# Performance work log

Measured on AMD Instinct MI355X. Metric: run time of the kernel, lower is better.

Reference implementation:

```python
import jax, jax.numpy as jnp
import numpy as np

HEAD = 8
PAD = (2, 2)   # (mod//2, mod//2 + mod%2) for dim=508, head=8 -> mod=4
EPS = 1e-6


def setup_inputs() -> dict:
    key = jax.random.key(0)
    ks = jax.random.split(key, 4)
    d_pad = 512  # 508 + mod(4)
    s = 1.0 / np.sqrt(d_pad).astype(np.float32)
    inp = jax.random.normal(ks[0], (2, 2048, 508), dtype=jnp.float32)
    Wq = jax.random.normal(ks[1], (d_pad, d_pad), dtype=jnp.float32) * s
    Wk = jax.random.normal(ks[2], (d_pad, d_pad), dtype=jnp.float32) * s
    Wv = jax.random.normal(ks[3], (d_pad, d_pad), dtype=jnp.float32) * s
    gamma = jnp.ones((d_pad,), dtype=jnp.float32)
    beta = jnp.zeros((d_pad,), dtype=jnp.float32)
    return {"inp": inp, "Wq": Wq, "Wk": Wk, "Wv": Wv, "gamma": gamma, "beta": beta}


def reference(inp, Wq, Wk, Wv, gamma, beta):
    # pad feature dim so it divides head count (torch F.pad on last dim)
    x = jnp.pad(inp, ((0, 0), (0, 0), (PAD[0], PAD[1])))  # [B, L, D]
    residual = x
    b, l, d = x.shape
    h = HEAD
    dh = d // h
    inv_sqrt_dh = 1.0 / np.sqrt(dh).astype(np.float32)

    def proj(W):
        # torch Linear (no bias): x @ W.T ; then split heads -> [B, H, L, dh]
        return (x @ W.T).reshape(b, l, h, dh).transpose(0, 2, 1, 3)

    q = proj(Wq)
    k = proj(Wk)
    v = proj(Wv)

    score = jnp.einsum('bhld,bhmd->bhlm', q, k) * inv_sqrt_dh  # [B,H,L,L]
    attn = jax.nn.softmax(score, axis=-1)
    out = jnp.einsum('bhlm,bhmd->bhld', attn, v)               # [B,H,L,dh]
    out = out.transpose(0, 2, 1, 3).reshape(b, l, d)           # unshape

    # dropout is identity in eval mode; residual + layernorm
    y = out + residual
    mu = jnp.mean(y, axis=-1, keepdims=True)
    var = jnp.mean(jnp.square(y - mu), axis=-1, keepdims=True)
    z = (y - mu) / jnp.sqrt(var + EPS)
    out = gamma * z + beta

    out = out[:, :, PAD[0]:-PAD[1]]  # strip padding back to original dim
    return out, attn
```

## Files before the change

kernel.cpp:

```cpp
#include <hip/hip_runtime.h>

typedef short bf16x8 __attribute__((ext_vector_type(8)));
typedef float f32x4 __attribute__((ext_vector_type(4)));
typedef unsigned short u16;
typedef u16 u16x8 __attribute__((ext_vector_type(8)));
typedef u16 u16x4 __attribute__((ext_vector_type(4)));

#define L_ 2048
#define D_ 512
#define H_ 8
#define DH_ 64
#define DIN 508

static __device__ __forceinline__ u16 f2b(float f){
  unsigned u = __builtin_bit_cast(unsigned, f);
  unsigned r = u + 0x7fffu + ((u >> 16) & 1u);
  return (u16)(r >> 16);
}
static __device__ __forceinline__ float b2f(u16 u){
  unsigned x = ((unsigned)u) << 16;
  return __builtin_bit_cast(float, x);
}
#define MFMA16(a,b,c) __builtin_amdgcn_mfma_f32_16x16x32_bf16(a,b,c,0,0,0)

__global__ __launch_bounds__(512) void proj_kernel(
    const float* __restrict__ inp, const float* __restrict__ Wq,
    const float* __restrict__ Wk, const float* __restrict__ Wv,
    u16* __restrict__ Qg, u16* __restrict__ Kg, u16* __restrict__ Vt)
{
  __shared__ u16 Xl[128*72];
  __shared__ u16 Wl[128*72];
  const int t = threadIdx.x;
  const int lane = t & 63, wid = t >> 6;
  const int wr = wid >> 2, wc = wid & 3;
  const int i0 = blockIdx.x * 128;
  const int j0 = blockIdx.y * 128;
  const int mat = j0 >> 9;
  const float* __restrict__ W = (mat==0) ? Wq : (mat==1) ? Wk : Wv;
  const int jbase = j0 & 511;
  const int srow = t >> 3, sc8 = (t & 7) * 8;

  f32x4 acc[4][2];
  #pragma unroll
  for (int a=0;a<4;++a){
    #pragma unroll
    for (int bq=0;bq<2;++bq){ f32x4 z = {0.f,0.f,0.f,0.f}; acc[a][bq] = z; }
  }

  for (int kt=0; kt<8; ++kt){
    const int k0 = kt*64;
    __syncthreads();
    #pragma unroll
    for (int it=0; it<2; ++it){
      const int r = srow + 64*it;
      u16x8 xb;
      const int gi = i0 + r;
      #pragma unroll
      for (int e=0;e<8;++e){
        const int k = k0 + sc8 + e;
        float v = (k>=2 && k<510) ? inp[gi*DIN + (k-2)] : 0.f;
        xb[e] = f2b(v);
      }
      *(u16x8*)&Xl[r*72 + sc8] = xb;
      const float* wp = W + (jbase + r)*D_ + k0 + sc8;
      u16x8 wb;
      #pragma unroll
      for (int e=0;e<8;++e) wb[e] = f2b(wp[e]);
      *(u16x8*)&Wl[r*72 + sc8] = wb;
    }
    __syncthreads();
    #pragma unroll
    for (int ks=0; ks<2; ++ks){
      const int ko = ks*32 + (lane>>4)*8;
      bf16x8 af[4], bfr[2];
      #pragma unroll
      for (int fm=0; fm<4; ++fm)
        af[fm] = *(const bf16x8*)&Xl[(wr*64 + fm*16 + (lane&15))*72 + ko];
      #pragma unroll
      for (int fn=0; fn<2; ++fn)
        bfr[fn] = *(const bf16x8*)&Wl[(wc*32 + fn*16 + (lane&15))*72 + ko];
      #pragma unroll
      for (int fm=0; fm<4; ++fm){
        #pragma unroll
        for (int fn=0; fn<2; ++fn)
          acc[fm][fn] = MFMA16(af[fm], bfr[fn], acc[fm][fn]);
      }
    }
  }
  #pragma unroll
  for (int fm=0; fm<4; ++fm){
    const int ibase = i0 + wr*64 + fm*16 + (lane>>4)*4;
    const int b = ibase >> 11;
    const int li = ibase & (L_-1);
    #pragma unroll
    for (int fn=0; fn<2; ++fn){
      const int n = j0 + wc*32 + fn*16 + (lane&15);
      const int h = (n>>6) & 7;
      const int dh = n & 63;
      if (mat == 2){
        u16x4 pk;
        #pragma unroll
        for (int r=0;r<4;++r) pk[r] = f2b(acc[fm][fn][r]);
        *(u16x4*)&Vt[((size_t)(b*H_+h)*DH_ + dh)*L_ + li] = pk;
      } else {
        u16* dst = ((mat==0)? Qg : Kg) + ((size_t)(b*H_+h)*L_ + li)*DH_ + dh;
        #pragma unroll
        for (int r=0;r<4;++r) dst[(size_t)r*DH_] = f2b(acc[fm][fn][r]);
      }
    }
  }
}

__global__ __launch_bounds__(512, 4) void attn_kernel(
    const u16* __restrict__ Qg, const u16* __restrict__ Kg,
    const u16* __restrict__ Vt, float* __restrict__ attn, float* __restrict__ Og)
{
  __shared__ u16 Kl[128*72];
  __shared__ u16 Vl[64*136];
  __shared__ u16 Pt[32*136];
  __shared__ float rsp[8][32];
  __shared__ float inv_rs[32];

  const int t = threadIdx.x, lane = t & 63, wid = t >> 6;
  const int q0 = blockIdx.x * 32;
  const int bh = blockIdx.y;
  const u16* Qp = Qg + ((size_t)bh*L_ + q0)*DH_;
  const u16* Kp = Kg + (size_t)bh*L_*DH_;
  const u16* Vp = Vt + (size_t)bh*DH_*L_;

  bf16x8 qf[2][2];
  #pragma unroll
  for (int qi=0;qi<2;++qi){
    #pragma unroll
    for (int ks=0;ks<2;++ks)
      qf[qi][ks] = *(const bf16x8*)&Qp[(size_t)(qi*16 + (lane&15))*DH_ + ks*32 + (lane>>4)*8];
  }

  const int kr0 = t>>3, kc8 = (t&7)*8;
  const int vr0 = t>>4, vcm = (t&15)*8;
  const int g4 = (lane>>4)*8;
  const int mrow = wid*16 + (lane&15);

  float racc0 = 0.f, racc1 = 0.f;
  u16x8 ka = *(const u16x8*)&Kp[(size_t)kr0*DH_ + kc8];
  u16x8 kb = *(const u16x8*)&Kp[(size_t)(64+kr0)*DH_ + kc8];
  for (int kt=0; kt<16; ++kt){
    __syncthreads();
    *(u16x8*)&Kl[kr0*72 + kc8] = ka;
    *(u16x8*)&Kl[(64+kr0)*72 + kc8] = kb;
    __syncthreads();
    if (kt < 15){
      ka = *(const u16x8*)&Kp[(size_t)((kt+1)*128 + kr0)*DH_ + kc8];
      kb = *(const u16x8*)&Kp[(size_t)((kt+1)*128 + 64 + kr0)*DH_ + kc8];
    }
    bf16x8 kf0 = *(const bf16x8*)&Kl[mrow*72 + g4];
    bf16x8 kf1 = *(const bf16x8*)&Kl[mrow*72 + 32 + g4];
    f32x4 s0 = {0.f,0.f,0.f,0.f}, s1 = {0.f,0.f,0.f,0.f};
    s0 = MFMA16(kf0, qf[0][0], s0); s0 = MFMA16(kf1, qf[0][1], s0);
    s1 = MFMA16(kf0, qf[1][0], s1); s1 = MFMA16(kf1, qf[1][1], s1);
    #pragma unroll
    for (int r=0;r<4;++r){
      racc0 += __expf(s0[r]*0.125f);
      racc1 += __expf(s1[r]*0.125f);
    }
  }
  racc0 += __shfl_xor(racc0, 16); racc0 += __shfl_xor(racc0, 32);
  racc1 += __shfl_xor(racc1, 16); racc1 += __shfl_xor(racc1, 32);
  if (lane < 16){ rsp[wid][lane] = racc0; rsp[wid][16+lane] = racc1; }
  __syncthreads();
  if (t < 32){
    float s = 0.f;
    #pragma unroll
    for (int w=0;w<8;++w) s += rsp[w][t];
    inv_rs[t] = 1.f/s;
  }
  __syncthreads();
  const float invq0 = inv_rs[lane&15];
  const float invq1 = inv_rs[16 + (lane&15)];

  const int qpv = wid>>2, d0 = (wid&3)*16;
  f32x4 o0 = {0.f,0.f,0.f,0.f}, o1 = {0.f,0.f,0.f,0.f};
  float* arow0 = attn + ((size_t)bh*L_ + q0 + (lane&15))*L_ + wid*16 + (lane>>4)*4;
  float* arow1 = arow0 + (size_t)16*L_;

  ka = *(const u16x8*)&Kp[(size_t)kr0*DH_ + kc8];
  kb = *(const u16x8*)&Kp[(size_t)(64+kr0)*DH_ + kc8];
  u16x8 va = *(const u16x8*)&Vp[(size_t)vr0*L_ + vcm];
  u16x8 vb = *(const u16x8*)&Vp[(size_t)(32+vr0)*L_ + vcm];
  for (int kt=0; kt<16; ++kt){
    __syncthreads();
    *(u16x8*)&Kl[kr0*72 + kc8] = ka;
    *(u16x8*)&Kl[(64+kr0)*72 + kc8] = kb;
    *(u16x8*)&Vl[vr0*136 + vcm] = va;
    *(u16x8*)&Vl[(32+vr0)*136 + vcm] = vb;
    __syncthreads();
    if (kt < 15){
      ka = *(const u16x8*)&Kp[(size_t)((kt+1)*128 + kr0)*DH_ + kc8];
      kb = *(const u16x8*)&Kp[(size_t)((kt+1)*128 + 64 + kr0)*DH_ + kc8];
      va = *(const u16x8*)&Vp[(size_t)vr0*L_ + (kt+1)*128 + vcm];
      vb = *(const u16x8*)&Vp[(size_t)(32+vr0)*L_ + (kt+1)*128 + vcm];
    }
    bf16x8 kf0 = *(const bf16x8*)&Kl[mrow*72 + g4];
    bf16x8 kf1 = *(const bf16x8*)&Kl[mrow*72 + 32 + g4];
    f32x4 s0 = {0.f,0.f,0.f,0.f}, s1 = {0.f,0.f,0.f,0.f};
    s0 = MFMA16(kf0, qf[0][0], s0); s0 = MFMA16(kf1, qf[0][1], s0);
    s1 = MFMA16(kf0, qf[1][0], s1); s1 = MFMA16(kf1, qf[1][1], s1);
    float4 a0, a1; u16x4 p0, p1;
    float e;
    e = __expf(s0[0]*0.125f); a0.x = e*invq0; p0[0] = f2b(e);
    e = __expf(s0[1]*0.125f); a0.y = e*invq0; p0[1] = f2b(e);
    e = __expf(s0[2]*0.125f); a0.z = e*invq0; p0[2] = f2b(e);
    e = __expf(s0[3]*0.125f); a0.w = e*invq0; p0[3] = f2b(e);
    e = __expf(s1[0]*0.125f); a1.x = e*invq1; p1[0] = f2b(e);
    e = __expf(s1[1]*0.125f); a1.y = e*invq1; p1[1] = f2b(e);
    e = __expf(s1[2]*0.125f); a1.z = e*invq1; p1[2] = f2b(e);
    e = __expf(s1[3]*0.125f); a1.w = e*invq1; p1[3] = f2b(e);
    *(float4*)&arow0[kt*128] = a0;
    *(float4*)&arow1[kt*128] = a1;
    *(u16x4*)&Pt[(lane&15)*136 + wid*16 + (lane>>4)*4] = p0;
    *(u16x4*)&Pt[(16 + (lane&15))*136 + wid*16 + (lane>>4)*4] = p1;
    __syncthreads();
    #pragma unroll
    for (int ms=0; ms<4; ++ms){
      bf16x8 pa = *(const bf16x8*)&Pt[(qpv*16 + (lane&15))*136 + ms*32 + g4];
      bf16x8 vv = *(const bf16x8*)&Vl[(d0 + (lane&15))*136 + ms*32 + g4];
      if (ms&1) o1 = MFMA16(pa, vv, o1); else o0 = MFMA16(pa, vv, o0);
    }
  }
  {
    const int b = bh>>3, h = bh&7;
    #pragma unroll
    for (int r=0;r<4;++r){
      const int qr = qpv*16 + (lane>>4)*4 + r;
      Og[((size_t)(b*L_ + q0 + qr))*D_ + h*DH_ + d0 + (lane&15)] = (o0[r]+o1[r])*inv_rs[qr];
    }
  }
}

__global__ __launch_bounds__(256) void ln_kernel(
    const float* __restrict__ Og, const float* __restrict__ inp,
    const float* __restrict__ gamma, const float* __restrict__ beta,
    float* __restrict__ out0)
{
  const int row = blockIdx.x, t = threadIdx.x;
  const int lane = t & 63, wid = t >> 6;
  const int c2 = t + 256;
  const float x1 = (t >= 2) ? inp[(size_t)row*DIN + t-2] : 0.f;
  const float x2 = (c2 < 510) ? inp[(size_t)row*DIN + c2-2] : 0.f;
  const float y1 = Og[(size_t)row*D_ + t]  + x1;
  const float y2 = Og[(size_t)row*D_ + c2] + x2;
  float s = y1 + y2, ss = y1*y1 + y2*y2;
  #pragma unroll
  for (int off=1; off<64; off<<=1){
    s  += __shfl_xor(s,  off);
    ss += __shfl_xor(ss, off);
  }
  __shared__ float red[4][2];
  if (lane == 0){ red[wid][0] = s; red[wid][1] = ss; }
  __syncthreads();
  s  = red[0][0]+red[1][0]+red[2][0]+red[3][0];
  ss = red[0][1]+red[1][1]+red[2][1]+red[3][1];
  const float mu   = s * (1.f/512.f);
  const float var  = ss * (1.f/512.f) - mu*mu;
  const float rstd = rsqrtf(var + 1e-6f);
  const float z1 = (y1 - mu)*rstd*gamma[t]  + beta[t];
  const float z2 = (y2 - mu)*rstd*gamma[c2] + beta[c2];
  if (t >= 2)   out0[(size_t)row*DIN + t-2]  = z1;
  if (c2 < 510) out0[(size_t)row*DIN + c2-2] = z2;
}

extern "C" void kernel_launch(void* const* d_in, const int* in_sizes, int n_in,
                              void* d_out, int out_size, void* d_ws, size_t ws_size,
                              hipStream_t stream) {
  const float* inp   = (const float*)d_in[0];
  const float* Wq    = (const float*)d_in[1];
  const float* Wk    = (const float*)d_in[2];
  const float* Wv    = (const float*)d_in[3];
  const float* gamma = (const float*)d_in[4];
  const float* beta  = (const float*)d_in[5];

  char* ws = (char*)d_ws;
  u16*   Qg = (u16*)(ws);
  u16*   Kg = (u16*)(ws + 4194304);
  u16*   Vt = (u16*)(ws + 8388608);
  float* Og = (float*)(ws + 12582912);

  float* out0 = (float*)d_out;
  float* attn = out0 + 2080768;

  proj_kernel<<<dim3(32,12), 512, 0, stream>>>(inp, Wq, Wk, Wv, Qg, Kg, Vt);
  attn_kernel<<<dim3(64,16), 512, 0, stream>>>(Qg, Kg, Vt, attn, Og);
  ln_kernel<<<4096, 256, 0, stream>>>(Og, inp, gamma, beta, out0);
}
```

Before: 129.3 us.

## Load K fragments directly from global and double-buffer V/P to cut barriers

K fragments for the score MFMAs are now read straight from global memory into registers, with a one-step prefetch, instead of being staged through shared memory. V and P tiles are double-buffered in shared memory so each iteration of the second pass needs one barrier instead of three. The attention-probability stores become nontemporal to avoid polluting cache. This trades shared-memory staging for less coalesced per-lane global K reads and more LDS use from the doubled buffers.

```diff
diff --git a/kernel.cpp b/kernel.cpp
--- a/kernel.cpp
+++ b/kernel.cpp
@@ -20,6 +20,9 @@
 static __device__ __forceinline__ float b2f(u16 u){
   unsigned x = ((unsigned)u) << 16;
   return __builtin_bit_cast(float, x);
+}
+static __device__ __forceinline__ bf16x8 asbf(u16x8 v){
+  return __builtin_bit_cast(bf16x8, v);
 }
 #define MFMA16(a,b,c) __builtin_amdgcn_mfma_f32_16x16x32_bf16(a,b,c,0,0,0)
 
@@ -115,11 +118,10 @@
     const u16* __restrict__ Qg, const u16* __restrict__ Kg,
     const u16* __restrict__ Vt, float* __restrict__ attn, float* __restrict__ Og)
 {
-  __shared__ u16 Kl[128*72];
-  __shared__ u16 Vl[64*136];
-  __shared__ u16 Pt[32*136];
-  __shared__ float rsp[8][32];
+  __shared__ u16 Vbuf[2*64*136];
+  __shared__ u16 Pbuf[2*32*136];
   __shared__ float inv_rs[32];
+  float* rsp = (float*)Vbuf;
 
   const int t = threadIdx.x, lane = t & 63, wid = t >> 6;
   const int q0 = blockIdx.x * 32;
@@ -136,42 +138,38 @@
       qf[qi][ks] = *(const bf16x8*)&Qp[(size_t)(qi*16 + (lane&15))*DH_ + ks*32 + (lane>>4)*8];
   }
 
-  const int kr0 = t>>3, kc8 = (t&7)*8;
   const int vr0 = t>>4, vcm = (t&15)*8;
   const int g4 = (lane>>4)*8;
   const int mrow = wid*16 + (lane&15);
 
   float racc0 = 0.f, racc1 = 0.f;
-  u16x8 ka = *(const u16x8*)&Kp[(size_t)kr0*DH_ + kc8];
-  u16x8 kb = *(const u16x8*)&Kp[(size_t)(64+kr0)*DH_ + kc8];
-  for (int kt=0; kt<16; ++kt){
-    __syncthreads();
-    *(u16x8*)&Kl[kr0*72 + kc8] = ka;
-    *(u16x8*)&Kl[(64+kr0)*72 + kc8] = kb;
-    __syncthreads();
-    if (kt < 15){
-      ka = *(const u16x8*)&Kp[(size_t)((kt+1)*128 + kr0)*DH_ + kc8];
-      kb = *(const u16x8*)&Kp[(size_t)((kt+1)*128 + 64 + kr0)*DH_ + kc8];
-    }
-    bf16x8 kf0 = *(const bf16x8*)&Kl[mrow*72 + g4];
-    bf16x8 kf1 = *(const bf16x8*)&Kl[mrow*72 + 32 + g4];
-    f32x4 s0 = {0.f,0.f,0.f,0.f}, s1 = {0.f,0.f,0.f,0.f};
-    s0 = MFMA16(kf0, qf[0][0], s0); s0 = MFMA16(kf1, qf[0][1], s0);
-    s1 = MFMA16(kf0, qf[1][0], s1); s1 = MFMA16(kf1, qf[1][1], s1);
-    #pragma unroll
-    for (int r=0;r<4;++r){
-      racc0 += __expf(s0[r]*0.125f);
-      racc1 += __expf(s1[r]*0.125f);
+  {
+    u16x8 nk0 = *(const u16x8*)&Kp[(size_t)mrow*DH_ + g4];
+    u16x8 nk1 = *(const u16x8*)&Kp[(size_t)mrow*DH_ + 32 + g4];
+    for (int kt=0; kt<16; ++kt){
+      bf16x8 kf0 = asbf(nk0), kf1 = asbf(nk1);
+      if (kt < 15){
+        nk0 = *(const u16x8*)&Kp[(size_t)((kt+1)*128 + mrow)*DH_ + g4];
+        nk1 = *(const u16x8*)&Kp[(size_t)((kt+1)*128 + mrow)*DH_ + 32 + g4];
+      }
+      f32x4 s0 = {0.f,0.f,0.f,0.f}, s1 = {0.f,0.f,0.f,0.f};
+      s0 = MFMA16(kf0, qf[0][0], s0); s0 = MFMA16(kf1, qf[0][1], s0);
+      s1 = MFMA16(kf0, qf[1][0], s1); s1 = MFMA16(kf1, qf[1][1], s1);
+      #pragma unroll
+      for (int r=0;r<4;++r){
+        racc0 += __expf(s0[r]*0.125f);
+        racc1 += __expf(s1[r]*0.125f);
+      }
     }
   }
   racc0 += __shfl_xor(racc0, 16); racc0 += __shfl_xor(racc0, 32);
   racc1 += __shfl_xor(racc1, 16); racc1 += __shfl_xor(racc1, 32);
-  if (lane < 16){ rsp[wid][lane] = racc0; rsp[wid][16+lane] = racc1; }
+  if (lane < 16){ rsp[wid*32 + lane] = racc0; rsp[wid*32 + 16 + lane] = racc1; }
   __syncthreads();
   if (t < 32){
     float s = 0.f;
     #pragma unroll
-    for (int w=0;w<8;++w) s += rsp[w][t];
+    for (int w=0;w<8;++w) s += rsp[w*32 + t];
     inv_rs[t] = 1.f/s;
   }
   __syncthreads();
@@ -183,47 +181,44 @@
   float* arow0 = attn + ((size_t)bh*L_ + q0 + (lane&15))*L_ + wid*16 + (lane>>4)*4;
   float* arow1 = arow0 + (size_t)16*L_;
 
-  ka = *(const u16x8*)&Kp[(size_t)kr0*DH_ + kc8];
-  kb = *(const u16x8*)&Kp[(size_t)(64+kr0)*DH_ + kc8];
+  u16x8 nk0 = *(const u16x8*)&Kp[(size_t)mrow*DH_ + g4];
+  u16x8 nk1 = *(const u16x8*)&Kp[(size_t)mrow*DH_ + 32 + g4];
   u16x8 va = *(const u16x8*)&Vp[(size_t)vr0*L_ + vcm];
   u16x8 vb = *(const u16x8*)&Vp[(size_t)(32+vr0)*L_ + vcm];
   for (int kt=0; kt<16; ++kt){
-    __syncthreads();
-    *(u16x8*)&Kl[kr0*72 + kc8] = ka;
-    *(u16x8*)&Kl[(64+kr0)*72 + kc8] = kb;
-    *(u16x8*)&Vl[vr0*136 + vcm] = va;
-    *(u16x8*)&Vl[(32+vr0)*136 + vcm] = vb;
-    __syncthreads();
-    if (kt < 15){
-      ka = *(const u16x8*)&Kp[(size_t)((kt+1)*128 + kr0)*DH_ + kc8];
-      kb = *(const u16x8*)&Kp[(size_t)((kt+1)*128 + 64 + kr0)*DH_ + kc8];
-      va = *(const u16x8*)&Vp[(size_t)vr0*L_ + (kt+1)*128 + vcm];
-      vb = *(const u16x8*)&Vp[(size_t)(32+vr0)*L_ + (kt+1)*128 + vcm];
-    }
-    bf16x8 kf0 = *(const bf16x8*)&Kl[mrow*72 + g4];
-    bf16x8 kf1 = *(const bf16x8*)&Kl[mrow*72 + 32 + g4];
+    u16* Vc = Vbuf + (kt&1)*64*136;
+    u16* Pc = Pbuf + (kt&1)*32*136;
+    *(u16x8*)&Vc[vr0*136 + vcm] = va;
+    *(u16x8*)&Vc[(32+vr0)*136 + vcm] = vb;
+    bf16x8 kf0 = asbf(nk0), kf1 = asbf(nk1);
     f32x4 s0 = {0.f,0.f,0.f,0.f}, s1 = {0.f,0.f,0.f,0.f};
     s0 = MFMA16(kf0, qf[0][0], s0); s0 = MFMA16(kf1, qf[0][1], s0);
     s1 = MFMA16(kf0, qf[1][0], s1); s1 = MFMA16(kf1, qf[1][1], s1);
-    float4 a0, a1; u16x4 p0, p1;
+    if (kt < 15){
+      nk0 = *(const u16x8*)&Kp[(size_t)((kt+1)*128 + mrow)*DH_ + g4];
+      nk1 = *(const u16x8*)&Kp[(size_t)((kt+1)*128 + mrow)*DH_ + 32 + g4];
+      va = *(const u16x8*)&Vp[(size_t)vr0*L_ + (kt+1)*128 + vcm];
+      vb = *(const u16x8*)&Vp[(size_t)(32+vr0)*L_ + (kt+1)*128 + vcm];
+    }
+    f32x4 a0, a1; u16x4 p0, p1;
     float e;
-    e = __expf(s0[0]*0.125f); a0.x = e*invq0; p0[0] = f2b(e);
-    e = __expf(s0[1]*0.125f); a0.y = e*invq0; p0[1] = f2b(e);
-    e = __expf(s0[2]*0.125f); a0.z = e*invq0; p0[2] = f2b(e);
-    e = __expf(s0[3]*0.125f); a0.w = e*invq0; p0[3] = f2b(e);
-    e = __expf(s1[0]*0.125f); a1.x = e*invq1; p1[0] = f2b(e);
-    e = __expf(s1[1]*0.125f); a1.y = e*invq1; p1[1] = f2b(e);
-    e = __expf(s1[2]*0.125f); a1.z = e*invq1; p1[2] = f2b(e);
-    e = __expf(s1[3]*0.125f); a1.w = e*invq1; p1[3] = f2b(e);
-    *(float4*)&arow0[kt*128] = a0;
-    *(float4*)&arow1[kt*128] = a1;
-    *(u16x4*)&Pt[(lane&15)*136 + wid*16 + (lane>>4)*4] = p0;
-    *(u16x4*)&Pt[(16 + (lane&15))*136 + wid*16 + (lane>>4)*4] = p1;
+    e = __expf(s0[0]*0.125f); a0[0] = e*invq0; p0[0] = f2b(e);
+    e = __expf(s0[1]*0.125f); a0[1] = e*invq0; p0[1] = f2b(e);
+    e = __expf(s0[2]*0.125f); a0[2] = e*invq0; p0[2] = f2b(e);
+    e = __expf(s0[3]*0.125f); a0[3] = e*invq0; p0[3] = f2b(e);
+    e = __expf(s1[0]*0.125f); a1[0] = e*invq1; p1[0] = f2b(e);
+    e = __expf(s1[1]*0.125f); a1[1] = e*invq1; p1[1] = f2b(e);
+    e = __expf(s1[2]*0.125f); a1[2] = e*invq1; p1[2] = f2b(e);
+    e = __expf(s1[3]*0.125f); a1[3] = e*invq1; p1[3] = f2b(e);
+    __builtin_nontemporal_store(a0, (f32x4*)&arow0[kt*128]);
+    __builtin_nontemporal_store(a1, (f32x4*)&arow1[kt*128]);
+    *(u16x4*)&Pc[(lane&15)*136 + wid*16 + (lane>>4)*4] = p0;
+    *(u16x4*)&Pc[(16 + (lane&15))*136 + wid*16 + (lane>>4)*4] = p1;
     __syncthreads();
     #pragma unroll
     for (int ms=0; ms<4; ++ms){
-      bf16x8 pa = *(const bf16x8*)&Pt[(qpv*16 + (lane&15))*136 + ms*32 + g4];
-      bf16x8 vv = *(const bf16x8*)&Vl[(d0 + (lane&15))*136 + ms*32 + g4];
+      bf16x8 pa = *(const bf16x8*)&Pc[(qpv*16 + (lane&15))*136 + ms*32 + g4];
+      bf16x8 vv = *(const bf16x8*)&Vc[(d0 + (lane&15))*136 + ms*32 + g4];
       if (ms&1) o1 = MFMA16(pa, vv, o1); else o0 = MFMA16(pa, vv, o0);
     }
   }
```

New measurement: 137.9 us. 6.7% more time.

## Pre-convert inputs to bf16, prefetch proj tiles, coalesce attention-probability stores

Applied to the files above, without the earlier changes.

A new conversion kernel pads the input and casts both the input and the weights to bf16 once. The projection GEMM then loads those bf16 tiles with register prefetch of the next K tile, instead of converting fp32 redundantly in every block. In the attention kernel, the normalized probability output is no longer written from each lane's MFMA fragment. It is read back row-wise from the bf16 P tile in shared memory and written as contiguous 32-byte nontemporal stores, to improve coalescing of the large attn output. The cost is one extra launch and a bf16-rounded attn output, which loses precision versus the previous fp32 values.

```diff
diff --git a/kernel.cpp b/kernel.cpp
--- a/kernel.cpp
+++ b/kernel.cpp
@@ -21,11 +21,42 @@
   unsigned x = ((unsigned)u) << 16;
   return __builtin_bit_cast(float, x);
 }
+static __device__ __forceinline__ bf16x8 asbf(u16x8 v){
+  return __builtin_bit_cast(bf16x8, v);
+}
 #define MFMA16(a,b,c) __builtin_amdgcn_mfma_f32_16x16x32_bf16(a,b,c,0,0,0)
 
-__global__ __launch_bounds__(512) void proj_kernel(
+__global__ __launch_bounds__(512) void cvt_kernel(
     const float* __restrict__ inp, const float* __restrict__ Wq,
     const float* __restrict__ Wk, const float* __restrict__ Wv,
+    u16* __restrict__ Xb, u16* __restrict__ Wb)
+{
+  const int tid = blockIdx.x*512 + threadIdx.x;
+  if (tid < 262144) {
+    const int idx8 = tid*8;
+    const int row = idx8 >> 9, col = idx8 & 511;
+    u16x8 o;
+    #pragma unroll
+    for (int e=0;e<8;++e){
+      const int c = col+e;
+      const float v = (c>=2 && c<510) ? inp[(size_t)row*DIN + (c-2)] : 0.f;
+      o[e] = f2b(v);
+    }
+    *(u16x8*)&Xb[idx8] = o;
+  } else {
+    const int idx8 = (tid - 262144)*8;
+    const int row = idx8 >> 9, col = idx8 & 511;
+    const float* __restrict__ W = (row < 512) ? Wq : (row < 1024) ? Wk : Wv;
+    const float* p = &W[(size_t)(row & 511)*D_ + col];
+    u16x8 o;
+    #pragma unroll
+    for (int e=0;e<8;++e) o[e] = f2b(p[e]);
+    *(u16x8*)&Wb[idx8] = o;
+  }
+}
+
+__global__ __launch_bounds__(512) void proj_kernel(
+    const u16* __restrict__ Xb, const u16* __restrict__ Wb,
     u16* __restrict__ Qg, u16* __restrict__ Kg, u16* __restrict__ Vt)
 {
   __shared__ u16 Xl[128*72];
@@ -36,8 +67,6 @@
   const int i0 = blockIdx.x * 128;
   const int j0 = blockIdx.y * 128;
   const int mat = j0 >> 9;
-  const float* __restrict__ W = (mat==0) ? Wq : (mat==1) ? Wk : Wv;
-  const int jbase = j0 & 511;
   const int srow = t >> 3, sc8 = (t & 7) * 8;
 
   f32x4 acc[4][2];
@@ -47,28 +76,25 @@
     for (int bq=0;bq<2;++bq){ f32x4 z = {0.f,0.f,0.f,0.f}; acc[a][bq] = z; }
   }
 
+  u16x8 xa0 = *(const u16x8*)&Xb[(size_t)(i0+srow)*D_ + sc8];
+  u16x8 xa1 = *(const u16x8*)&Xb[(size_t)(i0+64+srow)*D_ + sc8];
+  u16x8 wa0 = *(const u16x8*)&Wb[(size_t)(j0+srow)*D_ + sc8];
+  u16x8 wa1 = *(const u16x8*)&Wb[(size_t)(j0+64+srow)*D_ + sc8];
+
   for (int kt=0; kt<8; ++kt){
-    const int k0 = kt*64;
-    __syncthreads();
-    #pragma unroll
-    for (int it=0; it<2; ++it){
-      const int r = srow + 64*it;
-      u16x8 xb;
-      const int gi = i0 + r;
-      #pragma unroll
-      for (int e=0;e<8;++e){
-        const int k = k0 + sc8 + e;
-        float v = (k>=2 && k<510) ? inp[gi*DIN + (k-2)] : 0.f;
-        xb[e] = f2b(v);
-      }
-      *(u16x8*)&Xl[r*72 + sc8] = xb;
-      const float* wp = W + (jbase + r)*D_ + k0 + sc8;
-      u16x8 wb;
-      #pragma unroll
-      for (int e=0;e<8;++e) wb[e] = f2b(wp[e]);
-      *(u16x8*)&Wl[r*72 + sc8] = wb;
-    }
-    __syncthreads();
+    __syncthreads();
+    *(u16x8*)&Xl[srow*72 + sc8] = xa0;
+    *(u16x8*)&Xl[(64+srow)*72 + sc8] = xa1;
+    *(u16x8*)&Wl[srow*72 + sc8] = wa0;
+    *(u16x8*)&Wl[(64+srow)*72 + sc8] = wa1;
+    __syncthreads();
+    if (kt < 7){
+      const int k1 = (kt+1)*64;
+      xa0 = *(const u16x8*)&Xb[(size_t)(i0+srow)*D_ + k1 + sc8];
+      xa1 = *(const u16x8*)&Xb[(size_t)(i0+64+srow)*D_ + k1 + sc8];
+      wa0 = *(const u16x8*)&Wb[(size_t)(j0+srow)*D_ + k1 + sc8];
+      wa1 = *(const u16x8*)&Wb[(size_t)(j0+64+srow)*D_ + k1 + sc8];
+    }
     #pragma unroll
     for (int ks=0; ks<2; ++ks){
       const int ko = ks*32 + (lane>>4)*8;
@@ -175,13 +201,12 @@
     inv_rs[t] = 1.f/s;
   }
   __syncthreads();
-  const float invq0 = inv_rs[lane&15];
-  const float invq1 = inv_rs[16 + (lane&15)];
 
   const int qpv = wid>>2, d0 = (wid&3)*16;
   f32x4 o0 = {0.f,0.f,0.f,0.f}, o1 = {0.f,0.f,0.f,0.f};
-  float* arow0 = attn + ((size_t)bh*L_ + q0 + (lane&15))*L_ + wid*16 + (lane>>4)*4;
-  float* arow1 = arow0 + (size_t)16*L_;
+  const int sr = t >> 4;
+  const int sc = (t & 15) * 8;
+  float* abase = attn + ((size_t)bh*L_ + q0 + sr)*L_ + sc;
 
   ka = *(const u16x8*)&Kp[(size_t)kr0*DH_ + kc8];
   kb = *(const u16x8*)&Kp[(size_t)(64+kr0)*DH_ + kc8];
@@ -205,21 +230,25 @@
     f32x4 s0 = {0.f,0.f,0.f,0.f}, s1 = {0.f,0.f,0.f,0.f};
     s0 = MFMA16(kf0, qf[0][0], s0); s0 = MFMA16(kf1, qf[0][1], s0);
     s1 = MFMA16(kf0, qf[1][0], s1); s1 = MFMA16(kf1, qf[1][1], s1);
-    float4 a0, a1; u16x4 p0, p1;
-    float e;
-    e = __expf(s0[0]*0.125f); a0.x = e*invq0; p0[0] = f2b(e);
-    e = __expf(s0[1]*0.125f); a0.y = e*invq0; p0[1] = f2b(e);
-    e = __expf(s0[2]*0.125f); a0.z = e*invq0; p0[2] = f2b(e);
-    e = __expf(s0[3]*0.125f); a0.w = e*invq0; p0[3] = f2b(e);
-    e = __expf(s1[0]*0.125f); a1.x = e*invq1; p1[0] = f2b(e);
-    e = __expf(s1[1]*0.125f); a1.y = e*invq1; p1[1] = f2b(e);
-    e = __expf(s1[2]*0.125f); a1.z = e*invq1; p1[2] = f2b(e);
-    e = __expf(s1[3]*0.125f); a1.w = e*invq1; p1[3] = f2b(e);
-    *(float4*)&arow0[kt*128] = a0;
-    *(float4*)&arow1[kt*128] = a1;
+    u16x4 p0, p1;
+    p0[0] = f2b(__expf(s0[0]*0.125f)); p0[1] = f2b(__expf(s0[1]*0.125f));
+    p0[2] = f2b(__expf(s0[2]*0.125f)); p0[3] = f2b(__expf(s0[3]*0.125f));
+    p1[0] = f2b(__expf(s1[0]*0.125f)); p1[1] = f2b(__expf(s1[1]*0.125f));
+    p1[2] = f2b(__expf(s1[2]*0.125f)); p1[3] = f2b(__expf(s1[3]*0.125f));
     *(u16x4*)&Pt[(lane&15)*136 + wid*16 + (lane>>4)*4] = p0;
     *(u16x4*)&Pt[(16 + (lane&15))*136 + wid*16 + (lane>>4)*4] = p1;
     __syncthreads();
+    {
+      const u16x8 pv8 = *(const u16x8*)&Pt[sr*136 + sc];
+      const float inv = inv_rs[sr];
+      f32x4 w0, w1;
+      w0[0]=b2f(pv8[0])*inv; w0[1]=b2f(pv8[1])*inv;
+      w0[2]=b2f(pv8[2])*inv; w0[3]=b2f(pv8[3])*inv;
+      w1[0]=b2f(pv8[4])*inv; w1[1]=b2f(pv8[5])*inv;
+      w1[2]=b2f(pv8[6])*inv; w1[3]=b2f(pv8[7])*inv;
+      __builtin_nontemporal_store(w0, (f32x4*)&abase[kt*128]);
+      __builtin_nontemporal_store(w1, (f32x4*)&abase[kt*128 + 4]);
+    }
     #pragma unroll
     for (int ms=0; ms<4; ++ms){
       bf16x8 pa = *(const bf16x8*)&Pt[(qpv*16 + (lane&15))*136 + ms*32 + g4];
@@ -284,11 +313,14 @@
   u16*   Kg = (u16*)(ws + 4194304);
   u16*   Vt = (u16*)(ws + 8388608);
   float* Og = (float*)(ws + 12582912);
+  u16*   Xb = (u16*)(ws + 12582912);
+  u16*   Wb = (u16*)(ws + 16777216);
 
   float* out0 = (float*)d_out;
   float* attn = out0 + 2080768;
 
-  proj_kernel<<<dim3(32,12), 512, 0, stream>>>(inp, Wq, Wk, Wv, Qg, Kg, Vt);
+  cvt_kernel <<<704, 512, 0, stream>>>(inp, Wq, Wk, Wv, Xb, Wb);
+  proj_kernel<<<dim3(32,12), 512, 0, stream>>>(Xb, Wb, Qg, Kg, Vt);
   attn_kernel<<<dim3(64,16), 512, 0, stream>>>(Qg, Kg, Vt, attn, Og);
-  ln_kernel<<<4096, 256, 0, stream>>>(Og, inp, gamma, beta, out0);
-}
+  ln_kernel  <<<4096, 256, 0, stream>>>(Og, inp, gamma, beta, out0);
+}
```

After: 126.1 us. -2.5%, faster.
